# Kernel optimization log

Hardware: AMD Instinct MI355X
Metric: run time of the kernel (lower is better)

Reference implementation:

```python
import jax, jax.numpy as jnp
import numpy as np

EMBED_DIM = 2048
NUM_HEADS = 16
HEAD_DIM = EMBED_DIM // NUM_HEADS
BATCH = 4
SEQ = 1024
ROPE_BASE = 10000.0


def _rotate_half(x):
    x1, x2 = jnp.split(x, 2, axis=-1)
    return jnp.concatenate([-x2, x1], axis=-1)


def setup_inputs() -> dict:
    key = jax.random.key(0)
    ks = jax.random.split(key, 8)
    query = jax.random.normal(ks[0], (BATCH, SEQ, EMBED_DIM), dtype=jnp.float32)
    kkey = jax.random.normal(ks[1], (BATCH, SEQ, EMBED_DIM), dtype=jnp.float32)
    value = jax.random.normal(ks[2], (BATCH, SEQ, EMBED_DIM), dtype=jnp.float32)
    # causal mask: scores.masked_fill(mask == 0, -inf)
    mask = jnp.tril(jnp.ones((SEQ, SEQ), dtype=jnp.int32))[None, None]
    # RoPE tables [S, head_dim]
    inv_freq = 1.0 / (ROPE_BASE ** (np.arange(0, HEAD_DIM, 2, dtype=np.float32) / HEAD_DIM))
    pos = np.arange(SEQ, dtype=np.float32)
    freqs = np.outer(pos, inv_freq)                      # [S, D/2]
    emb = np.concatenate([freqs, freqs], axis=-1)        # [S, D]
    rope_cos = jnp.asarray(np.cos(emb), dtype=jnp.float32)
    rope_sin = jnp.asarray(np.sin(emb), dtype=jnp.float32)
    s = 1.0 / np.sqrt(EMBED_DIM)
    Wq = jax.random.normal(ks[3], (EMBED_DIM, EMBED_DIM), dtype=jnp.float32) * s
    Wk = jax.random.normal(ks[4], (EMBED_DIM, EMBED_DIM), dtype=jnp.float32) * s
    Wv = jax.random.normal(ks[5], (EMBED_DIM, EMBED_DIM), dtype=jnp.float32) * s
    Wo = jax.random.normal(ks[6], (EMBED_DIM, EMBED_DIM), dtype=jnp.float32) * s
    return {"query": query, "key": kkey, "value": value, "mask": mask,
            "rope_cos": rope_cos, "rope_sin": rope_sin,
            "Wq": Wq, "Wk": Wk, "Wv": Wv, "Wo": Wo}


def reference(query, key, value, mask, rope_cos, rope_sin, Wq, Wk, Wv, Wo):
    B, S, E = query.shape
    # projections (nn.Linear: x @ W.T)
    def proj(x, W):
        y = x @ W.T
        return y.reshape(B, -1, NUM_HEADS, HEAD_DIM).transpose(0, 2, 1, 3)  # [B,H,S,D]
    Q = proj(query, Wq)
    K = proj(key, Wk)
    V = proj(value, Wv)
    # RoPE (rotate-half form), cos/sin broadcast over batch and heads
    cos = rope_cos[None, None]  # [1,1,S,D]
    sin = rope_sin[None, None]
    Q = Q * cos + _rotate_half(Q) * sin
    K = K * cos + _rotate_half(K) * sin
    scale = jnp.asarray(np.sqrt(HEAD_DIM), dtype=Q.dtype)
    scores = jnp.einsum('bhqd,bhkd->bhqk', Q, K) / scale
    scores = jnp.where(mask == 0, jnp.asarray(-jnp.inf, scores.dtype), scores)
    attn = jax.nn.softmax(scores, axis=-1)
    context = jnp.einsum('bhqk,bhkd->bhqd', attn, V)
    context = context.transpose(0, 2, 1, 3).reshape(B, S, E)
    out = context @ Wo.T
    return out
```

## Files before the change

### kernel.cpp

```cpp
#include <hip/hip_runtime.h>
#include <stdint.h>

#define E_DIM 2048
#define N_HEADS 16
#define H_DIM 128
#define BATCH 4
#define SEQL 1024
#define M_ROWS 4096

typedef __attribute__((ext_vector_type(8))) short bf16x8;
typedef __attribute__((ext_vector_type(4))) float f32x4;

#define AS1 __attribute__((address_space(1)))
#define AS3 __attribute__((address_space(3)))

__device__ __forceinline__ void gload16(const void* g, void* l) {
  __builtin_amdgcn_global_load_lds((const AS1 uint32_t*)g, (AS3 uint32_t*)l, 16, 0, 0);
}

__device__ __forceinline__ unsigned short f2bf(float f) {
  union { float f; uint32_t u; } v; v.f = f;
  return (unsigned short)((v.u + 0x7FFFu + ((v.u >> 16) & 1u)) >> 16);
}

__global__ __launch_bounds__(256) void k_cvtx(const float* __restrict__ a,
                                              const float* __restrict__ b,
                                              const float* __restrict__ c,
                                              ushort* __restrict__ oa,
                                              ushort* __restrict__ ob,
                                              ushort* __restrict__ oc) {
  int which = blockIdx.y;
  const float* in = (which == 0) ? a : (which == 1) ? b : c;
  ushort* out = (which == 0) ? oa : (which == 1) ? ob : oc;
  int i = (blockIdx.x * 256 + threadIdx.x) * 4;
  float4 v = *reinterpret_cast<const float4*>(in + i);
  *reinterpret_cast<ushort4*>(out + i) =
      make_ushort4(f2bf(v.x), f2bf(v.y), f2bf(v.z), f2bf(v.w));
}

__global__ __launch_bounds__(256) void k_cvtw(const float* __restrict__ a,
                                              const float* __restrict__ b,
                                              const float* __restrict__ c,
                                              const float* __restrict__ d,
                                              ushort* __restrict__ oa,
                                              ushort* __restrict__ ob,
                                              ushort* __restrict__ oc,
                                              ushort* __restrict__ od) {
  int which = blockIdx.y;
  const float* in = (which == 0) ? a : (which == 1) ? b : (which == 2) ? c : d;
  ushort* out = (which == 0) ? oa : (which == 1) ? ob : (which == 2) ? oc : od;
  int i = (blockIdx.x * 256 + threadIdx.x) * 4;
  float4 v = *reinterpret_cast<const float4*>(in + i);
  *reinterpret_cast<ushort4*>(out + i) =
      make_ushort4(f2bf(v.x), f2bf(v.y), f2bf(v.z), f2bf(v.w));
}

__device__ __forceinline__ void gemm_mainloop(const ushort* __restrict__ A,
                                              const ushort* __restrict__ W,
                                              ushort* As, ushort* Bs,
                                              int m0, int n0,
                                              const int browRows[4],
                                              f32x4 (&acc)[4][4]) {
  const int tid = threadIdx.x;
  const int w = tid >> 6, lane = tid & 63, quad = lane >> 4, lid = lane & 15;
  const int wm = (w & 1) * 64;

  const int g0 = tid, g1 = tid + 256;
  const int r0 = g0 >> 2, j0 = (g0 & 3) ^ ((r0 >> 1) & 3);
  const int r1 = g1 >> 2, j1 = (g1 & 3) ^ ((r1 >> 1) & 3);
  const ushort* gA0 = A + (size_t)(m0 + r0) * E_DIM + j0 * 8;
  const ushort* gA1 = A + (size_t)(m0 + r1) * E_DIM + j1 * 8;
  const ushort* gB0 = W + (size_t)(n0 + r0) * E_DIM + j0 * 8;
  const ushort* gB1 = W + (size_t)(n0 + r1) * E_DIM + j1 * 8;
  ushort* lA0 = As + (w * 64) * 8;
  ushort* lA1 = As + (256 + w * 64) * 8;
  ushort* lB0 = Bs + (w * 64) * 8;
  ushort* lB1 = Bs + (256 + w * 64) * 8;

  const ushort* aAddr[4];
  const ushort* bAddr[4];
  for (int mi = 0; mi < 4; ++mi) {
    int row = wm + mi * 16 + lid;
    aAddr[mi] = As + row * 32 + ((quad ^ ((row >> 1) & 3)) * 8);
  }
  for (int ni = 0; ni < 4; ++ni) {
    int row = browRows[ni];
    bAddr[ni] = Bs + row * 32 + ((quad ^ ((row >> 1) & 3)) * 8);
  }

  for (int k = 0; k < E_DIM; k += 32) {
    __syncthreads();
    gload16(gA0, lA0); gload16(gA1, lA1);
    gload16(gB0, lB0); gload16(gB1, lB1);
    gA0 += 32; gA1 += 32; gB0 += 32; gB1 += 32;
    __syncthreads();
    bf16x8 af[4], bfr[4];
    for (int mi = 0; mi < 4; ++mi) af[mi] = *reinterpret_cast<const bf16x8*>(aAddr[mi]);
    for (int ni = 0; ni < 4; ++ni) bfr[ni] = *reinterpret_cast<const bf16x8*>(bAddr[ni]);
    for (int mi = 0; mi < 4; ++mi)
      for (int ni = 0; ni < 4; ++ni)
        acc[mi][ni] = __builtin_amdgcn_mfma_f32_16x16x32_bf16(af[mi], bfr[ni], acc[mi][ni], 0, 0, 0);
  }
}

__global__ __launch_bounds__(256) void k_gemm_qkv(
    const ushort* __restrict__ xq, const ushort* __restrict__ xk, const ushort* __restrict__ xv,
    const ushort* __restrict__ wq, const ushort* __restrict__ wk, const ushort* __restrict__ wv,
    ushort* __restrict__ Qr, ushort* __restrict__ Kr, ushort* __restrict__ Vr,
    const float* __restrict__ cosT, const float* __restrict__ sinT) {
  __shared__ ushort As[128 * 32];
  __shared__ ushort Bs[128 * 32];
  const int z = blockIdx.z;
  const ushort* A = (z == 0) ? xq : (z == 1) ? xk : xv;
  const ushort* W = (z == 0) ? wq : (z == 1) ? wk : wv;
  ushort* Out = (z == 0) ? Qr : (z == 1) ? Kr : Vr;
  const int tid = threadIdx.x;
  const int w = tid >> 6, lane = tid & 63, quad = lane >> 4, lid = lane & 15;
  const int n0 = blockIdx.x * 128;
  const int m0 = blockIdx.y * 128;
  const int wm = (w & 1) * 64;

  int colrow[4];
  for (int ni = 0; ni < 4; ++ni)
    colrow[ni] = (w >> 1) * 32 + (ni & 1) * 16 + (ni >> 1) * 64 + lid;

  f32x4 acc[4][4];
  const f32x4 z4 = {0.f, 0.f, 0.f, 0.f};
  for (int i = 0; i < 4; ++i)
    for (int j = 0; j < 4; ++j) acc[i][j] = z4;

  gemm_mainloop(A, W, As, Bs, m0, n0, colrow, acc);

  const int b = m0 >> 10;
  const int h = n0 >> 7;
  ushort* Og = Out + (size_t)(b * N_HEADS + h) * SEQL * H_DIM;
  const bool rope = (z < 2);
  for (int mi = 0; mi < 4; ++mi)
    for (int r = 0; r < 4; ++r) {
      int s = (m0 & (SEQL - 1)) + wm + mi * 16 + quad * 4 + r;
      size_t row = (size_t)s * H_DIM;
      if (rope) {
        for (int ni = 0; ni < 2; ++ni) {
          int d0 = (w >> 1) * 32 + ni * 16 + lid;
          float c = cosT[s * H_DIM + d0];
          float sn = sinT[s * H_DIM + d0];
          float x0 = acc[mi][ni][r], x1 = acc[mi][ni + 2][r];
          Og[row + d0]      = f2bf(x0 * c - x1 * sn);
          Og[row + d0 + 64] = f2bf(x1 * c + x0 * sn);
        }
      } else {
        for (int ni = 0; ni < 4; ++ni)
          Og[row + colrow[ni]] = f2bf(acc[mi][ni][r]);
      }
    }
}

__global__ __launch_bounds__(256) void k_gemm_o(const ushort* __restrict__ A,
                                                const ushort* __restrict__ W,
                                                float* __restrict__ Out) {
  __shared__ ushort As[128 * 32];
  __shared__ ushort Bs[128 * 32];
  const int tid = threadIdx.x;
  const int w = tid >> 6, lane = tid & 63, quad = lane >> 4, lid = lane & 15;
  const int n0 = blockIdx.x * 128;
  const int m0 = blockIdx.y * 128;
  const int wm = (w & 1) * 64;

  int colrow[4];
  for (int ni = 0; ni < 4; ++ni) colrow[ni] = (w >> 1) * 64 + ni * 16 + lid;

  f32x4 acc[4][4];
  const f32x4 z4 = {0.f, 0.f, 0.f, 0.f};
  for (int i = 0; i < 4; ++i)
    for (int j = 0; j < 4; ++j) acc[i][j] = z4;

  gemm_mainloop(A, W, As, Bs, m0, n0, colrow, acc);

  for (int mi = 0; mi < 4; ++mi)
    for (int r = 0; r < 4; ++r) {
      size_t row = (size_t)(m0 + wm + mi * 16 + quad * 4 + r) * E_DIM + n0;
      for (int ni = 0; ni < 4; ++ni) Out[row + colrow[ni]] = acc[mi][ni][r];
    }
}

__global__ __launch_bounds__(256) void k_transv(const ushort* __restrict__ V,
                                                ushort* __restrict__ Vt) {
  __shared__ ushort t[32][33];
  int bh = blockIdx.z;
  int s0 = blockIdx.x * 32;
  int d0 = blockIdx.y * 32;
  int j = threadIdx.x & 31;
  int i = threadIdx.x >> 5;
  for (int rr = 0; rr < 4; ++rr) {
    int row = i + rr * 8;
    t[row][j] = V[((size_t)bh * SEQL + s0 + row) * H_DIM + d0 + j];
  }
  __syncthreads();
  for (int rr = 0; rr < 4; ++rr) {
    int drow = i + rr * 8;
    Vt[((size_t)bh * H_DIM + d0 + drow) * SEQL + s0 + j] = t[j][drow];
  }
}

__global__ __launch_bounds__(256, 2) void k_attn(const ushort* __restrict__ Q,
                                                 const ushort* __restrict__ K,
                                                 const ushort* __restrict__ Vt,
                                                 ushort* __restrict__ Ctx) {
  __shared__ ushort Ks[128 * 128];
  __shared__ ushort Vs[128 * 64];
  __shared__ ushort Ps[4][32 * 40];
  const int tid = threadIdx.x;
  const int w = tid >> 6, lane = tid & 63, quad = lane >> 4, lid = lane & 15;
  const int l = blockIdx.y * 8 + blockIdx.x;
  const int bh = l & 63;
  const int slot = l >> 6;
  const int qt = (slot < 4) ? slot : 11 - slot;
  const int q0 = qt * 128;
  const size_t base = (size_t)bh * SEQL * H_DIM;
  const ushort* Qg = Q + base;
  const ushort* Kg = K + base;
  const ushort* Vg = Vt + base;

  bf16x8 qf[2][4];
  for (int mt = 0; mt < 2; ++mt) {
    int row = q0 + w * 32 + mt * 16 + lid;
    for (int kc = 0; kc < 4; ++kc)
      qf[mt][kc] = *reinterpret_cast<const bf16x8*>(Qg + (size_t)row * H_DIM + kc * 32 + quad * 8);
  }

  f32x4 oacc[2][8];
  f32x4 lacc[2];
  const f32x4 z4 = {0.f, 0.f, 0.f, 0.f};
  for (int mt = 0; mt < 2; ++mt) {
    lacc[mt] = z4;
    for (int dt = 0; dt < 8; ++dt) oacc[mt][dt] = z4;
  }

  bf16x8 ones;
  for (int i = 0; i < 8; ++i) ones[i] = (short)0x3F80;

  const float SC2 = 0.08838834764831845f * 1.4426950408889634f;
  const float M2 = 12.0f * 1.4426950408889634f;

  for (int j0 = 0; j0 <= q0; j0 += 128) {
    const bool diag = (j0 == q0);
    __syncthreads();
    for (int i = 0; i < 8; ++i) {
      int g = i * 256 + tid;
      int kk = g >> 4;
      int c = (g & 15) ^ (kk & 15);
      gload16(Kg + (size_t)(j0 + kk) * H_DIM + c * 8, Ks + (i * 256 + w * 64) * 8);
    }
    for (int i = 0; i < 4; ++i) {
      int g = i * 256 + tid;
      int d = g >> 3;
      int c = (g & 7) ^ (d & 7);
      gload16(Vg + (size_t)d * SEQL + j0 + c * 8, Vs + (i * 256 + w * 64) * 8);
    }
    __syncthreads();

    f32x4 sacc[2][8];
    for (int mt = 0; mt < 2; ++mt)
      for (int nt = 0; nt < 8; ++nt) sacc[mt][nt] = z4;
    for (int kc = 0; kc < 4; ++kc)
      for (int nt = 0; nt < 8; ++nt) {
        int kk = nt * 16 + lid;
        bf16x8 kf = *reinterpret_cast<const bf16x8*>(
            Ks + kk * H_DIM + (((kc * 4 + quad) ^ lid) * 8));
        sacc[0][nt] = __builtin_amdgcn_mfma_f32_16x16x32_bf16(qf[0][kc], kf, sacc[0][nt], 0, 0, 0);
        sacc[1][nt] = __builtin_amdgcn_mfma_f32_16x16x32_bf16(qf[1][kc], kf, sacc[1][nt], 0, 0, 0);
      }

    if (diag) {
      for (int mt = 0; mt < 2; ++mt)
        for (int nt = 0; nt < 8; ++nt)
          for (int r = 0; r < 4; ++r) {
            int key = j0 + nt * 16 + lid;
            int row = q0 + w * 32 + mt * 16 + quad * 4 + r;
            if (key > row) sacc[mt][nt][r] = -3.0e38f;
          }
    }

    ushort* Pw = Ps[w];
    for (int kc = 0; kc < 4; ++kc) {
      if (kc == 2) {
        __syncthreads();
        for (int i = 0; i < 4; ++i) {
          int g = i * 256 + tid;
          int d = g >> 3;
          int c = (g & 7) ^ (d & 7);
          gload16(Vg + (size_t)d * SEQL + j0 + 64 + c * 8, Vs + (i * 256 + w * 64) * 8);
        }
        __syncthreads();
      }
      for (int mt = 0; mt < 2; ++mt)
        for (int half = 0; half < 2; ++half) {
          int nt = kc * 2 + half;
          for (int r = 0; r < 4; ++r) {
            float p = exp2f(fmaf(sacc[mt][nt][r], SC2, -M2));
            Pw[(mt * 16 + quad * 4 + r) * 40 + half * 16 + lid] = f2bf(p);
          }
        }
      bf16x8 pf0 = *reinterpret_cast<const bf16x8*>(Pw + lid * 40 + quad * 8);
      bf16x8 pf1 = *reinterpret_cast<const bf16x8*>(Pw + (16 + lid) * 40 + quad * 8);
      lacc[0] = __builtin_amdgcn_mfma_f32_16x16x32_bf16(pf0, ones, lacc[0], 0, 0, 0);
      lacc[1] = __builtin_amdgcn_mfma_f32_16x16x32_bf16(pf1, ones, lacc[1], 0, 0, 0);
      int kcl = kc & 1;
      for (int dt = 0; dt < 8; ++dt) {
        int d = dt * 16 + lid;
        bf16x8 vf = *reinterpret_cast<const bf16x8*>(
            Vs + d * 64 + (((kcl * 4 + quad) ^ (d & 7)) * 8));
        oacc[0][dt] = __builtin_amdgcn_mfma_f32_16x16x32_bf16(pf0, vf, oacc[0][dt], 0, 0, 0);
        oacc[1][dt] = __builtin_amdgcn_mfma_f32_16x16x32_bf16(pf1, vf, oacc[1][dt], 0, 0, 0);
      }
    }
  }

  const int b = bh >> 4, h = bh & 15;
  for (int mt = 0; mt < 2; ++mt)
    for (int r = 0; r < 4; ++r) {
      int s = q0 + w * 32 + mt * 16 + quad * 4 + r;
      float inv = 1.0f / lacc[mt][r];
      for (int dt = 0; dt < 8; ++dt)
        Ctx[(size_t)(b * SEQL + s) * E_DIM + h * H_DIM + dt * 16 + lid] =
            f2bf(oacc[mt][dt][r] * inv);
    }
}

extern "C" void kernel_launch(void* const* d_in, const int* in_sizes, int n_in,
                              void* d_out, int out_size, void* d_ws, size_t ws_size,
                              hipStream_t stream) {
  const float* q_in = (const float*)d_in[0];
  const float* k_in = (const float*)d_in[1];
  const float* v_in = (const float*)d_in[2];
  const float* rc = (const float*)d_in[4];
  const float* rs = (const float*)d_in[5];
  const float* Wq = (const float*)d_in[6];
  const float* Wk = (const float*)d_in[7];
  const float* Wv = (const float*)d_in[8];
  const float* Wo = (const float*)d_in[9];
  float* out = (float*)d_out;

  ushort* p = (ushort*)d_ws;
  const size_t WSZ = (size_t)E_DIM * E_DIM;
  const size_t XSZ = (size_t)M_ROWS * E_DIM;
  ushort* wq_b = p; p += WSZ;
  ushort* wk_b = p; p += WSZ;
  ushort* wv_b = p; p += WSZ;
  ushort* wo_b = p; p += WSZ;
  ushort* xq_b = p; p += XSZ;
  ushort* xk_b = p; p += XSZ;
  ushort* xv_b = p; p += XSZ;
  ushort* Qr = p;   p += XSZ;
  ushort* Kr = p;   p += XSZ;
  ushort* Vr = p;   p += XSZ;
  ushort* Vt = p;   p += XSZ;
  ushort* ctx = xq_b;

  dim3 blk(256);
  k_cvtx<<<dim3((unsigned)(XSZ / 1024), 3), blk, 0, stream>>>(q_in, k_in, v_in, xq_b, xk_b, xv_b);
  k_cvtw<<<dim3((unsigned)(WSZ / 1024), 4), blk, 0, stream>>>(Wq, Wk, Wv, Wo, wq_b, wk_b, wv_b, wo_b);

  k_gemm_qkv<<<dim3(E_DIM / 128, M_ROWS / 128, 3), blk, 0, stream>>>(
      xq_b, xk_b, xv_b, wq_b, wk_b, wv_b, Qr, Kr, Vr, rc, rs);

  k_transv<<<dim3(SEQL / 32, H_DIM / 32, BATCH * N_HEADS), blk, 0, stream>>>(Vr, Vt);

  k_attn<<<dim3(8, BATCH * N_HEADS), blk, 0, stream>>>(Qr, Kr, Vt, ctx);

  k_gemm_o<<<dim3(E_DIM / 128, M_ROWS / 128), blk, 0, stream>>>(ctx, wo_b, out);
}
```

Measured before the change: 432.1 us.

## Widen GEMM K-step, fuse V transpose into QKV epilogue, halve attention K tile

The shared GEMM mainloop now loads 64-wide K slices per iteration with an 8-way XOR swizzle, which halves the number of barrier pairs. The V projection epilogue transposes its tile through shared memory and writes V^T directly, so the separate transpose kernel and its intermediate buffer go away. The attention kernel loads the K tile in two 64-row halves to cut LDS use and raises the launch-bounds occupancy hint from 2 to 3 blocks, at the cost of an extra barrier pair per key block.

```diff
diff --git a/kernel.cpp b/kernel.cpp
--- a/kernel.cpp
+++ b/kernel.cpp
@@ -55,65 +55,77 @@
       make_ushort4(f2bf(v.x), f2bf(v.y), f2bf(v.z), f2bf(v.w));
 }
 
-__device__ __forceinline__ void gemm_mainloop(const ushort* __restrict__ A,
-                                              const ushort* __restrict__ W,
-                                              ushort* As, ushort* Bs,
-                                              int m0, int n0,
-                                              const int browRows[4],
-                                              f32x4 (&acc)[4][4]) {
+__device__ __forceinline__ void gemm_mainloop64(const ushort* __restrict__ A,
+                                                const ushort* __restrict__ W,
+                                                ushort* As, ushort* Bs,
+                                                int m0, int n0,
+                                                const int browRows[4],
+                                                f32x4 (&acc)[4][4]) {
   const int tid = threadIdx.x;
   const int w = tid >> 6, lane = tid & 63, quad = lane >> 4, lid = lane & 15;
   const int wm = (w & 1) * 64;
 
-  const int g0 = tid, g1 = tid + 256;
-  const int r0 = g0 >> 2, j0 = (g0 & 3) ^ ((r0 >> 1) & 3);
-  const int r1 = g1 >> 2, j1 = (g1 & 3) ^ ((r1 >> 1) & 3);
-  const ushort* gA0 = A + (size_t)(m0 + r0) * E_DIM + j0 * 8;
-  const ushort* gA1 = A + (size_t)(m0 + r1) * E_DIM + j1 * 8;
-  const ushort* gB0 = W + (size_t)(n0 + r0) * E_DIM + j0 * 8;
-  const ushort* gB1 = W + (size_t)(n0 + r1) * E_DIM + j1 * 8;
-  ushort* lA0 = As + (w * 64) * 8;
-  ushort* lA1 = As + (256 + w * 64) * 8;
-  ushort* lB0 = Bs + (w * 64) * 8;
-  ushort* lB1 = Bs + (256 + w * 64) * 8;
+  const ushort* gA[4];
+  const ushort* gB[4];
+  ushort* lA[4];
+  ushort* lB[4];
+  for (int i = 0; i < 4; ++i) {
+    int g = i * 256 + tid;
+    int r = g >> 3;
+    int c = (g & 7) ^ (r & 7);
+    gA[i] = A + (size_t)(m0 + r) * E_DIM + c * 8;
+    gB[i] = W + (size_t)(n0 + r) * E_DIM + c * 8;
+    lA[i] = As + (i * 256 + w * 64) * 8;
+    lB[i] = Bs + (i * 256 + w * 64) * 8;
+  }
 
   const ushort* aAddr[4];
   const ushort* bAddr[4];
   for (int mi = 0; mi < 4; ++mi) {
     int row = wm + mi * 16 + lid;
-    aAddr[mi] = As + row * 32 + ((quad ^ ((row >> 1) & 3)) * 8);
+    aAddr[mi] = As + row * 64 + ((quad ^ (row & 7)) * 8);
   }
   for (int ni = 0; ni < 4; ++ni) {
     int row = browRows[ni];
-    bAddr[ni] = Bs + row * 32 + ((quad ^ ((row >> 1) & 3)) * 8);
-  }
-
-  for (int k = 0; k < E_DIM; k += 32) {
-    __syncthreads();
-    gload16(gA0, lA0); gload16(gA1, lA1);
-    gload16(gB0, lB0); gload16(gB1, lB1);
-    gA0 += 32; gA1 += 32; gB0 += 32; gB1 += 32;
-    __syncthreads();
-    bf16x8 af[4], bfr[4];
-    for (int mi = 0; mi < 4; ++mi) af[mi] = *reinterpret_cast<const bf16x8*>(aAddr[mi]);
-    for (int ni = 0; ni < 4; ++ni) bfr[ni] = *reinterpret_cast<const bf16x8*>(bAddr[ni]);
-    for (int mi = 0; mi < 4; ++mi)
+    bAddr[ni] = Bs + row * 64 + ((quad ^ (row & 7)) * 8);
+  }
+
+  for (int k = 0; k < E_DIM; k += 64) {
+    __syncthreads();
+    for (int i = 0; i < 4; ++i) {
+      gload16(gA[i], lA[i]);
+      gload16(gB[i], lB[i]);
+      gA[i] += 64;
+      gB[i] += 64;
+    }
+    __syncthreads();
+    for (int kc = 0; kc < 2; ++kc) {
+      bf16x8 af[4], bfr[4];
+      for (int mi = 0; mi < 4; ++mi)
+        af[mi] = *reinterpret_cast<const bf16x8*>(
+            (const ushort*)((uintptr_t)aAddr[mi] ^ (uintptr_t)(kc * 64)));
       for (int ni = 0; ni < 4; ++ni)
-        acc[mi][ni] = __builtin_amdgcn_mfma_f32_16x16x32_bf16(af[mi], bfr[ni], acc[mi][ni], 0, 0, 0);
+        bfr[ni] = *reinterpret_cast<const bf16x8*>(
+            (const ushort*)((uintptr_t)bAddr[ni] ^ (uintptr_t)(kc * 64)));
+      for (int mi = 0; mi < 4; ++mi)
+        for (int ni = 0; ni < 4; ++ni)
+          acc[mi][ni] =
+              __builtin_amdgcn_mfma_f32_16x16x32_bf16(af[mi], bfr[ni], acc[mi][ni], 0, 0, 0);
+    }
   }
 }
 
 __global__ __launch_bounds__(256) void k_gemm_qkv(
     const ushort* __restrict__ xq, const ushort* __restrict__ xk, const ushort* __restrict__ xv,
     const ushort* __restrict__ wq, const ushort* __restrict__ wk, const ushort* __restrict__ wv,
-    ushort* __restrict__ Qr, ushort* __restrict__ Kr, ushort* __restrict__ Vr,
+    ushort* __restrict__ Qr, ushort* __restrict__ Kr, ushort* __restrict__ Vt,
     const float* __restrict__ cosT, const float* __restrict__ sinT) {
-  __shared__ ushort As[128 * 32];
-  __shared__ ushort Bs[128 * 32];
+  __shared__ ushort smem[2 * 128 * 64];
+  ushort* As = smem;
+  ushort* Bs = smem + 128 * 64;
   const int z = blockIdx.z;
   const ushort* A = (z == 0) ? xq : (z == 1) ? xk : xv;
   const ushort* W = (z == 0) ? wq : (z == 1) ? wk : wv;
-  ushort* Out = (z == 0) ? Qr : (z == 1) ? Kr : Vr;
   const int tid = threadIdx.x;
   const int w = tid >> 6, lane = tid & 63, quad = lane >> 4, lid = lane & 15;
   const int n0 = blockIdx.x * 128;
@@ -121,25 +133,28 @@
   const int wm = (w & 1) * 64;
 
   int colrow[4];
-  for (int ni = 0; ni < 4; ++ni)
-    colrow[ni] = (w >> 1) * 32 + (ni & 1) * 16 + (ni >> 1) * 64 + lid;
+  if (z < 2) {
+    for (int ni = 0; ni < 4; ++ni)
+      colrow[ni] = (w >> 1) * 32 + (ni & 1) * 16 + (ni >> 1) * 64 + lid;
+  } else {
+    for (int ni = 0; ni < 4; ++ni) colrow[ni] = (w >> 1) * 64 + ni * 16 + lid;
+  }
 
   f32x4 acc[4][4];
   const f32x4 z4 = {0.f, 0.f, 0.f, 0.f};
   for (int i = 0; i < 4; ++i)
     for (int j = 0; j < 4; ++j) acc[i][j] = z4;
 
-  gemm_mainloop(A, W, As, Bs, m0, n0, colrow, acc);
+  gemm_mainloop64(A, W, As, Bs, m0, n0, colrow, acc);
 
   const int b = m0 >> 10;
   const int h = n0 >> 7;
-  ushort* Og = Out + (size_t)(b * N_HEADS + h) * SEQL * H_DIM;
-  const bool rope = (z < 2);
-  for (int mi = 0; mi < 4; ++mi)
-    for (int r = 0; r < 4; ++r) {
-      int s = (m0 & (SEQL - 1)) + wm + mi * 16 + quad * 4 + r;
-      size_t row = (size_t)s * H_DIM;
-      if (rope) {
+  if (z < 2) {
+    ushort* Og = ((z == 0) ? Qr : Kr) + (size_t)(b * N_HEADS + h) * SEQL * H_DIM;
+    for (int mi = 0; mi < 4; ++mi)
+      for (int r = 0; r < 4; ++r) {
+        int s = (m0 & (SEQL - 1)) + wm + mi * 16 + quad * 4 + r;
+        size_t row = (size_t)s * H_DIM;
         for (int ni = 0; ni < 2; ++ni) {
           int d0 = (w >> 1) * 32 + ni * 16 + lid;
           float c = cosT[s * H_DIM + d0];
@@ -148,18 +163,41 @@
           Og[row + d0]      = f2bf(x0 * c - x1 * sn);
           Og[row + d0 + 64] = f2bf(x1 * c + x0 * sn);
         }
-      } else {
-        for (int ni = 0; ni < 4; ++ni)
-          Og[row + colrow[ni]] = f2bf(acc[mi][ni][r]);
-      }
-    }
+      }
+  } else {
+    const int TS = 136;
+    ushort* T = smem;
+    ushort* Vg = Vt + (size_t)(b * N_HEADS + h) * H_DIM * SEQL;
+    const int s0 = m0 & (SEQL - 1);
+    for (int ch = 0; ch < 2; ++ch) {
+      __syncthreads();
+      if ((w >> 1) == ch) {
+        for (int mi = 0; mi < 4; ++mi)
+          for (int ni = 0; ni < 4; ++ni) {
+            int dl = ni * 16 + lid;
+            for (int r = 0; r < 4; ++r) {
+              int sl = wm + mi * 16 + quad * 4 + r;
+              T[dl * TS + sl] = f2bf(acc[mi][ni][r]);
+            }
+          }
+      }
+      __syncthreads();
+      int dl = tid >> 2;
+      for (int pass = 0; pass < 4; ++pass) {
+        int c = (tid & 3) + pass * 4;
+        bf16x8 v = *reinterpret_cast<const bf16x8*>(T + dl * TS + c * 8);
+        *reinterpret_cast<bf16x8*>(Vg + (size_t)(ch * 64 + dl) * SEQL + s0 + c * 8) = v;
+      }
+    }
+  }
 }
 
 __global__ __launch_bounds__(256) void k_gemm_o(const ushort* __restrict__ A,
                                                 const ushort* __restrict__ W,
                                                 float* __restrict__ Out) {
-  __shared__ ushort As[128 * 32];
-  __shared__ ushort Bs[128 * 32];
+  __shared__ ushort smem[2 * 128 * 64];
+  ushort* As = smem;
+  ushort* Bs = smem + 128 * 64;
   const int tid = threadIdx.x;
   const int w = tid >> 6, lane = tid & 63, quad = lane >> 4, lid = lane & 15;
   const int n0 = blockIdx.x * 128;
@@ -174,7 +212,7 @@
   for (int i = 0; i < 4; ++i)
     for (int j = 0; j < 4; ++j) acc[i][j] = z4;
 
-  gemm_mainloop(A, W, As, Bs, m0, n0, colrow, acc);
+  gemm_mainloop64(A, W, As, Bs, m0, n0, colrow, acc);
 
   for (int mi = 0; mi < 4; ++mi)
     for (int r = 0; r < 4; ++r) {
@@ -183,30 +221,11 @@
     }
 }
 
-__global__ __launch_bounds__(256) void k_transv(const ushort* __restrict__ V,
-                                                ushort* __restrict__ Vt) {
-  __shared__ ushort t[32][33];
-  int bh = blockIdx.z;
-  int s0 = blockIdx.x * 32;
-  int d0 = blockIdx.y * 32;
-  int j = threadIdx.x & 31;
-  int i = threadIdx.x >> 5;
-  for (int rr = 0; rr < 4; ++rr) {
-    int row = i + rr * 8;
-    t[row][j] = V[((size_t)bh * SEQL + s0 + row) * H_DIM + d0 + j];
-  }
-  __syncthreads();
-  for (int rr = 0; rr < 4; ++rr) {
-    int drow = i + rr * 8;
-    Vt[((size_t)bh * H_DIM + d0 + drow) * SEQL + s0 + j] = t[j][drow];
-  }
-}
-
-__global__ __launch_bounds__(256, 2) void k_attn(const ushort* __restrict__ Q,
+__global__ __launch_bounds__(256, 3) void k_attn(const ushort* __restrict__ Q,
                                                  const ushort* __restrict__ K,
                                                  const ushort* __restrict__ Vt,
                                                  ushort* __restrict__ Ctx) {
-  __shared__ ushort Ks[128 * 128];
+  __shared__ ushort Ks[64 * 128];
   __shared__ ushort Vs[128 * 64];
   __shared__ ushort Ps[4][32 * 40];
   const int tid = threadIdx.x;
@@ -244,8 +263,12 @@
 
   for (int j0 = 0; j0 <= q0; j0 += 128) {
     const bool diag = (j0 == q0);
-    __syncthreads();
-    for (int i = 0; i < 8; ++i) {
+    f32x4 sacc[2][8];
+    for (int mt = 0; mt < 2; ++mt)
+      for (int nt = 0; nt < 8; ++nt) sacc[mt][nt] = z4;
+
+    __syncthreads();
+    for (int i = 0; i < 4; ++i) {
       int g = i * 256 + tid;
       int kk = g >> 4;
       int c = (g & 15) ^ (kk & 15);
@@ -259,16 +282,33 @@
     }
     __syncthreads();
 
-    f32x4 sacc[2][8];
-    for (int mt = 0; mt < 2; ++mt)
-      for (int nt = 0; nt < 8; ++nt) sacc[mt][nt] = z4;
     for (int kc = 0; kc < 4; ++kc)
-      for (int nt = 0; nt < 8; ++nt) {
-        int kk = nt * 16 + lid;
+      for (int ntl = 0; ntl < 4; ++ntl) {
+        int kk = ntl * 16 + lid;
         bf16x8 kf = *reinterpret_cast<const bf16x8*>(
             Ks + kk * H_DIM + (((kc * 4 + quad) ^ lid) * 8));
-        sacc[0][nt] = __builtin_amdgcn_mfma_f32_16x16x32_bf16(qf[0][kc], kf, sacc[0][nt], 0, 0, 0);
-        sacc[1][nt] = __builtin_amdgcn_mfma_f32_16x16x32_bf16(qf[1][kc], kf, sacc[1][nt], 0, 0, 0);
+        sacc[0][ntl] = __builtin_amdgcn_mfma_f32_16x16x32_bf16(qf[0][kc], kf, sacc[0][ntl], 0, 0, 0);
+        sacc[1][ntl] = __builtin_amdgcn_mfma_f32_16x16x32_bf16(qf[1][kc], kf, sacc[1][ntl], 0, 0, 0);
+      }
+
+    __syncthreads();
+    for (int i = 0; i < 4; ++i) {
+      int g = i * 256 + tid;
+      int kk = g >> 4;
+      int c = (g & 15) ^ (kk & 15);
+      gload16(Kg + (size_t)(j0 + 64 + kk) * H_DIM + c * 8, Ks + (i * 256 + w * 64) * 8);
+    }
+    __syncthreads();
+
+    for (int kc = 0; kc < 4; ++kc)
+      for (int ntl = 0; ntl < 4; ++ntl) {
+        int kk = ntl * 16 + lid;
+        bf16x8 kf = *reinterpret_cast<const bf16x8*>(
+            Ks + kk * H_DIM + (((kc * 4 + quad) ^ lid) * 8));
+        sacc[0][4 + ntl] =
+            __builtin_amdgcn_mfma_f32_16x16x32_bf16(qf[0][kc], kf, sacc[0][4 + ntl], 0, 0, 0);
+        sacc[1][4 + ntl] =
+            __builtin_amdgcn_mfma_f32_16x16x32_bf16(qf[1][kc], kf, sacc[1][4 + ntl], 0, 0, 0);
       }
 
     if (diag) {
@@ -353,7 +393,6 @@
   ushort* xv_b = p; p += XSZ;
   ushort* Qr = p;   p += XSZ;
   ushort* Kr = p;   p += XSZ;
-  ushort* Vr = p;   p += XSZ;
   ushort* Vt = p;   p += XSZ;
   ushort* ctx = xq_b;
 
@@ -362,9 +401,7 @@
   k_cvtw<<<dim3((unsigned)(WSZ / 1024), 4), blk, 0, stream>>>(Wq, Wk, Wv, Wo, wq_b, wk_b, wv_b, wo_b);
 
   k_gemm_qkv<<<dim3(E_DIM / 128, M_ROWS / 128, 3), blk, 0, stream>>>(
-      xq_b, xk_b, xv_b, wq_b, wk_b, wv_b, Qr, Kr, Vr, rc, rs);
-
-  k_transv<<<dim3(SEQL / 32, H_DIM / 32, BATCH * N_HEADS), blk, 0, stream>>>(Vr, Vt);
+      xq_b, xk_b, xv_b, wq_b, wk_b, wv_b, Qr, Kr, Vt, rc, rs);
 
   k_attn<<<dim3(8, BATCH * N_HEADS), blk, 0, stream>>>(Qr, Kr, Vt, ctx);
 
```

Measured after the change: 582.8 us. 1.35x slower.
